# Kernel tuning notes

Hardware: AMD Instinct MI355X
Metric: run time of the kernel (lower is better)

The kernel has to match this reference:

```python
import jax, jax.numpy as jnp
import numpy as np

N, L, H, D = 4, 8192, 8, 64  # batch, seq len, heads, per-head dim
DIM = H * D


def _log_exp_kernel(x):
    # log(1 + exp(x)) positive feature map (softplus)
    return jax.nn.softplus(x)


def setup_inputs() -> dict:
    key = jax.random.key(0)
    k0, k1, k2, k3, k4 = jax.random.split(key, 5)
    s = 1.0 / np.sqrt(DIM).astype(np.float32)
    return {
        "query": jax.random.normal(k0, (N, L, DIM), jnp.float32),
        "key": jax.random.normal(k1, (N, L, DIM), jnp.float32),
        "Wq": jax.random.normal(k2, (DIM, DIM), jnp.float32) * s,
        "Wk": jax.random.normal(k3, (DIM, DIM), jnp.float32) * s,
        "Wv": jax.random.normal(k4, (DIM, DIM), jnp.float32) * s,
    }


def _causal_linear_attention(q, k, v):
    # q, k: (N,H,L,D) kernelized features; v: (N,H,L,D)
    # out[t] = (q_t . S_t) / (q_t . z_t), S_t = sum_{s<=t} k_s v_s^T, z_t = sum_{s<=t} k_s
    qs = jnp.moveaxis(q, 2, 0)  # (L,N,H,D)
    ks = jnp.moveaxis(k, 2, 0)
    vs = jnp.moveaxis(v, 2, 0)
    S0 = jnp.zeros((q.shape[0], q.shape[1], q.shape[3], v.shape[3]), q.dtype)
    z0 = jnp.zeros((q.shape[0], q.shape[1], q.shape[3]), q.dtype)

    def step(carry, xs):
        S, z = carry
        qt, kt, vt = xs  # each (N,H,D)
        S = S + kt[..., :, None] * vt[..., None, :]  # (N,H,D,D)
        z = z + kt
        num = jnp.einsum('nhd,nhde->nhe', qt, S)
        den = jnp.einsum('nhd,nhd->nh', qt, z)
        return (S, z), num / den[..., None]

    _, out = jax.lax.scan(step, (S0, z0), (qs, ks, vs))  # out: (L,N,H,D)
    return jnp.moveaxis(out, 0, 2)  # (N,H,L,D)


def reference(query, key, Wq, Wk, Wv):
    n, Lq, dim = query.shape
    # projections (torch Linear, no bias: x @ W.T), kernel applied in forward...
    q = _log_exp_kernel(query @ Wq.T).reshape(n, Lq, H, D).transpose(0, 2, 1, 3)
    k = _log_exp_kernel(key @ Wk.T).reshape(n, Lq, H, D).transpose(0, 2, 1, 3)
    v = (key @ Wv.T).reshape(n, Lq, H, D).transpose(0, 2, 1, 3)
    # ...and again inside _attention_linear (faithful to the source)
    q = _log_exp_kernel(q)
    k = _log_exp_kernel(k)
    att = _causal_linear_attention(q, k, v)  # (N,H,L,D)
    return att.transpose(0, 2, 1, 3).reshape(n, Lq, H * D)
```

## Files before the change

kernel.cpp:

```cpp
#include <hip/hip_runtime.h>


using bf16x8 = __attribute__((ext_vector_type(8))) short;
using u16x8  = __attribute__((ext_vector_type(8))) unsigned short;
using f32x4  = __attribute__((ext_vector_type(4))) float;

#define L_SEQ   8192
#define NCHUNK  128
#define RECB    8448

__device__ __forceinline__ float bf2f(unsigned short u) {
  union { unsigned int i; float f; } c; c.i = ((unsigned int)u) << 16; return c.f;
}
__device__ __forceinline__ unsigned short f2bf(float f) {
  union { float f; unsigned int i; } c; c.f = f;
  unsigned int r = c.i + 0x7fffu + ((c.i >> 16) & 1u);
  return (unsigned short)(r >> 16);
}
__device__ __forceinline__ float sp_(float x) {
  return (x > 20.0f) ? x : __logf(1.0f + __expf(x));
}
__device__ __forceinline__ void gll16(const void* g, void* l) {
  __builtin_amdgcn_global_load_lds(
      (const __attribute__((address_space(1))) unsigned int*)g,
      (__attribute__((address_space(3))) unsigned int*)l, 16, 0, 0);
}

__global__ void cvt_all(const float* __restrict__ q, const float* __restrict__ k,
                        const float* __restrict__ wq, const float* __restrict__ wk,
                        const float* __restrict__ wv,
                        unsigned short* __restrict__ qo, unsigned short* __restrict__ ko,
                        unsigned short* __restrict__ wqo, unsigned short* __restrict__ wko,
                        unsigned short* __restrict__ wvo) {
  const int stride = gridDim.x * blockDim.x;
  for (int i = blockIdx.x * blockDim.x + threadIdx.x; i < 8585216; i += stride) {
    const float* src; unsigned short* dst; int off;
    if (i < 4194304)      { src = q;  dst = qo;  off = i; }
    else if (i < 8388608) { src = k;  dst = ko;  off = i - 4194304; }
    else if (i < 8454144) { src = wq; dst = wqo; off = i - 8388608; }
    else if (i < 8519680) { src = wk; dst = wko; off = i - 8454144; }
    else                  { src = wv; dst = wvo; off = i - 8519680; }
    float4 v = ((const float4*)src)[off];
    ushort4 o;
    o.x = f2bf(v.x); o.y = f2bf(v.y); o.z = f2bf(v.z); o.w = f2bf(v.w);
    ((ushort4*)dst)[off] = o;
  }
}

__global__ __launch_bounds__(512, 2) void gemm_stream(const unsigned short* __restrict__ qbf,
                                                      const unsigned short* __restrict__ kbf,
                                                      const unsigned short* __restrict__ wqb,
                                                      const unsigned short* __restrict__ wkb,
                                                      const unsigned short* __restrict__ wvb,
                                                      unsigned short* __restrict__ qb,
                                                      unsigned short* __restrict__ kb,
                                                      unsigned short* __restrict__ vt) {
  __shared__ char Ws[131072];
  const int g = blockIdx.x, sub = g >> 8, b = g & 255;
  const int xcd = b & 7, t = b >> 3;
  const int bm = (xcd + (t >> 2) * 8) * 512;
  const int bn = (t & 3) * 128;

  const unsigned short* A; const unsigned short* W; unsigned short* outp; int mode;
  if (sub == 0)      { A = qbf; W = wqb; outp = qb; mode = 0; }
  else if (sub == 1) { A = kbf; W = wkb; outp = kb; mode = 0; }
  else               { A = kbf; W = wvb; outp = vt; mode = 1; }

  const int tid = threadIdx.x, lane = tid & 63, wv = tid >> 6;
  const int l15 = lane & 15, lg = lane >> 4;

  const char* Wb = (const char*)W;
#pragma unroll
  for (int it = 0; it < 16; ++it) {
    const int p = it * 8192 + tid * 16;
    const int col = p >> 10, kb2 = p & 1023;
    gll16(Wb + (size_t)(bn + col) * 1024 + (kb2 ^ ((col & 7) << 4)),
          Ws + it * 8192 + wv * 1024);
  }
  __syncthreads();

  const char* Ab = (const char*)A + (size_t)(bm + wv * 64 + l15) * 1024 + lg * 16;

  f32x4 acc[4][8] = {};
  bf16x8 aC[4], aN[4];
#pragma unroll
  for (int rg = 0; rg < 4; ++rg) aC[rg] = *(const bf16x8*)(Ab + rg * 16384);

#pragma unroll 1
  for (int kk = 0; kk < 16; ++kk) {
    if (kk < 15) {
#pragma unroll
      for (int rg = 0; rg < 4; ++rg)
        aN[rg] = *(const bf16x8*)(Ab + rg * 16384 + (kk + 1) * 64);
    }
    bf16x8 bf[8];
#pragma unroll
    for (int cf = 0; cf < 8; ++cf) {
      const int col = cf * 16 + l15;
      bf[cf] = *(const bf16x8*)(Ws + col * 1024 + ((kk * 64 + lg * 16) ^ ((col & 7) << 4)));
    }
#pragma unroll
    for (int rg = 0; rg < 4; ++rg)
#pragma unroll
      for (int cf = 0; cf < 8; ++cf)
        acc[rg][cf] = __builtin_amdgcn_mfma_f32_16x16x32_bf16(aC[rg], bf[cf], acc[rg][cf], 0, 0, 0);
    if (kk < 15) {
#pragma unroll
      for (int rg = 0; rg < 4; ++rg) aC[rg] = aN[rg];
    }
  }

#pragma unroll
  for (int rg = 0; rg < 4; ++rg)
#pragma unroll
    for (int cf = 0; cf < 8; ++cf)
#pragma unroll
      for (int j = 0; j < 4; ++j) {
        const int m = bm + wv * 64 + rg * 16 + lg * 4 + j;
        const int n = bn + cf * 16 + l15;
        float x = acc[rg][cf][j];
        const int nb = m >> 13;
        const int l  = m & 8191;
        const int h  = n >> 6;
        if (mode == 0) {
          x = sp_(sp_(x));
          const int d = n & 63;
          outp[(((size_t)(nb * 8 + h) * 8192 + l) << 6) + d] = f2bf(x);
        } else {
          const int e = n & 63;
          const int cc = l >> 6, s = l & 63;
          outp[(((size_t)((nb * 8 + h) * 128 + cc) * 64 + e) << 6) + s] = f2bf(x);
        }
      }
}

__global__ __launch_bounds__(256, 4) void chunk_sums(const unsigned short* __restrict__ kb,
                                                     const unsigned short* __restrict__ vt,
                                                     char* __restrict__ S) {
  const int b  = blockIdx.x;
  const int nh = b >> 7, c = b & 127;
  __shared__ char Kt[8192];
  __shared__ char STs[8192];
  const int tid = threadIdx.x, lane = tid & 63, wave = tid >> 6;
  const int l15 = lane & 15, lg = lane >> 4;
  const unsigned short* kch = kb + ((size_t)(nh * L_SEQ + c * 64) << 6);
  const unsigned short* vch = vt + ((size_t)b << 12);

  {
    const int s = tid >> 2, d0 = (tid & 3) << 4;
    u16x8 a = *(const u16x8*)(kch + s * 64 + d0);
    u16x8 bb = *(const u16x8*)(kch + s * 64 + d0 + 8);
#pragma unroll
    for (int i = 0; i < 8; ++i) {
      const int d = d0 + i;
      *(unsigned short*)(Kt + d * 128 + ((2 * s) ^ ((d & 7) << 4))) = a[i];
    }
#pragma unroll
    for (int i = 0; i < 8; ++i) {
      const int d = d0 + 8 + i;
      *(unsigned short*)(Kt + d * 128 + ((2 * s) ^ ((d & 7) << 4))) = bb[i];
    }
  }
  __syncthreads();

  f32x4 acc[4] = {};
#pragma unroll
  for (int kk = 0; kk < 2; ++kk) {
    bf16x8 av = *(const bf16x8*)(vch + (wave * 16 + l15) * 64 + kk * 32 + lg * 8);
#pragma unroll
    for (int ni = 0; ni < 4; ++ni) {
      const int d = ni * 16 + l15;
      bf16x8 bk = *(const bf16x8*)(Kt + d * 128 + ((kk * 64 + lg * 16) ^ ((d & 7) << 4)));
      acc[ni] = __builtin_amdgcn_mfma_f32_16x16x32_bf16(av, bk, acc[ni], 0, 0, 0);
    }
  }

  char* rec = S + (size_t)b * RECB;

  if (tid < 64) {
    float z = 0.f;
#pragma unroll
    for (int kk = 0; kk < 8; ++kk) {
      bf16x8 kv = *(const bf16x8*)(Kt + tid * 128 + ((kk * 16) ^ ((tid & 7) << 4)));
#pragma unroll
      for (int i = 0; i < 8; ++i) z += bf2f(kv[i]);
    }
    *(float*)(rec + 8192 + tid * 4) = z;
  }

#pragma unroll
  for (int ni = 0; ni < 4; ++ni)
#pragma unroll
    for (int j = 0; j < 4; ++j) {
      const int e = wave * 16 + lg * 4 + j, d = ni * 16 + l15;
      *(unsigned short*)(STs + e * 128 + d * 2) = f2bf(acc[ni][j]);
    }
  __syncthreads();
  {
    const int off = tid * 32;
    *(u16x8*)(rec + off)      = *(const u16x8*)(STs + off);
    *(u16x8*)(rec + off + 16) = *(const u16x8*)(STs + off + 16);
  }
}

__global__ void scan_chunks(char* __restrict__ S) {
  const int g = blockIdx.x * 256 + threadIdx.x;
  if (g < 65536) {
    const int nh = g >> 11, pr = g & 2047;
    char* p = S + (size_t)nh * NCHUNK * RECB + pr * 4;
    float a0 = 0.f, a1 = 0.f;
    for (int c = 0; c < NCHUNK; ++c) {
      const unsigned int u = *(unsigned int*)p;
      const float t0 = bf2f((unsigned short)(u & 0xffff));
      const float t1 = bf2f((unsigned short)(u >> 16));
      *(unsigned int*)p = (unsigned int)f2bf(a0) | ((unsigned int)f2bf(a1) << 16);
      a0 += t0; a1 += t1;
      p += RECB;
    }
  } else if (g < 67584) {
    const int idx = g - 65536;
    const int nh = idx >> 6, d = idx & 63;
    char* p = S + (size_t)nh * NCHUNK * RECB + 8192 + d * 4;
    float a = 0.f;
    for (int c = 0; c < NCHUNK; ++c) {
      const float t = *(float*)p; *(float*)p = a; a += t; p += RECB;
    }
  }
}

__global__ __launch_bounds__(256, 2) void attn_out(const unsigned short* __restrict__ qb,
                                                   const unsigned short* __restrict__ kb,
                                                   const unsigned short* __restrict__ vt,
                                                   const char* __restrict__ S,
                                                   float* __restrict__ out) {
  const int b  = blockIdx.x;
  const int nh = b >> 7, c = b & 127;
  const int nb = nh >> 3, h = nh & 7;
  __shared__ char Qs[8192], Ks[8192], Vs[8192], STs[8192], Ps[8192];
  __shared__ float zsh[64], dzh[64];
  const int tid = threadIdx.x, lane = tid & 63, wave = tid >> 6;
  const int l15 = lane & 15, lg = lane >> 4;

  const char* qch = (const char*)(qb + ((size_t)(nh * L_SEQ + c * 64) << 6));
  const char* kch = (const char*)(kb + ((size_t)(nh * L_SEQ + c * 64) << 6));
  const char* vch = (const char*)(vt + ((size_t)b << 12));
  const char* rb  = S + (size_t)b * RECB;

#pragma unroll
  for (int it = 0; it < 2; ++it) {
    const int p  = wave * 2048 + it * 1024 + lane * 16;
    const int r  = p >> 7;
    const int cb = (p & 127) ^ ((r & 7) << 4);
    const int src = r * 128 + cb;
    gll16(qch + src, Qs + wave * 2048 + it * 1024);
    gll16(kch + src, Ks + wave * 2048 + it * 1024);
    gll16(vch + src, Vs + wave * 2048 + it * 1024);
    gll16(rb + src,  STs + wave * 2048 + it * 1024);
  }
  if (tid < 64) zsh[tid] = *(const float*)(rb + 8192 + tid * 4);
  __syncthreads();

  {
    const int t = tid >> 2, p4 = tid & 3;
    float dq = 0.f;
#pragma unroll
    for (int half = 0; half < 2; ++half) {
      const int d0 = p4 * 16 + half * 8;
      const int cb = (d0 * 2) ^ ((t & 7) << 4);
      u16x8 qv = *(const u16x8*)(Qs + t * 128 + cb);
#pragma unroll
      for (int i = 0; i < 8; ++i) dq += bf2f(qv[i]) * zsh[d0 + i];
    }
    dq += __shfl_xor(dq, 1);
    dq += __shfl_xor(dq, 2);
    if (p4 == 0) dzh[t] = dq;
  }
  __syncthreads();

  f32x4 accA[4] = {};
#pragma unroll
  for (int kk = 0; kk < 2; ++kk) {
    const int cb = kk * 64 + lg * 16;
    const int rq = wave * 16 + l15;
    bf16x8 aq = *(const bf16x8*)(Qs + rq * 128 + (cb ^ ((rq & 7) << 4)));
#pragma unroll
    for (int ni = 0; ni < 4; ++ni) {
      const int rk = ni * 16 + l15;
      bf16x8 bk = *(const bf16x8*)(Ks + rk * 128 + (cb ^ ((rk & 7) << 4)));
      accA[ni] = __builtin_amdgcn_mfma_f32_16x16x32_bf16(aq, bk, accA[ni], 0, 0, 0);
    }
  }

  float den4[4];
#pragma unroll
  for (int j = 0; j < 4; ++j) {
    const int t = wave * 16 + lg * 4 + j;
    float rs = 0.f;
#pragma unroll
    for (int ni = 0; ni < 4; ++ni) {
      const int s = ni * 16 + l15;
      const float v = (s <= t) ? accA[ni][j] : 0.f;
      const unsigned short pb = f2bf(v);
      rs += bf2f(pb);
      *(unsigned short*)(Ps + t * 128 + ((s * 2) ^ ((t & 7) << 4))) = pb;
    }
    rs += __shfl_xor(rs, 1);
    rs += __shfl_xor(rs, 2);
    rs += __shfl_xor(rs, 4);
    rs += __shfl_xor(rs, 8);
    den4[j] = rs + dzh[t];
  }
  __syncthreads();

  f32x4 accO[4] = {};
#pragma unroll
  for (int kk = 0; kk < 2; ++kk) {
    const int cb = kk * 64 + lg * 16;
    const int rp = wave * 16 + l15;
    bf16x8 ap = *(const bf16x8*)(Ps + rp * 128 + (cb ^ ((rp & 7) << 4)));
    bf16x8 aq = *(const bf16x8*)(Qs + rp * 128 + (cb ^ ((rp & 7) << 4)));
#pragma unroll
    for (int ni = 0; ni < 4; ++ni) {
      const int rv = ni * 16 + l15;
      bf16x8 bv = *(const bf16x8*)(Vs + rv * 128 + (cb ^ ((rv & 7) << 4)));
      bf16x8 bs = *(const bf16x8*)(STs + rv * 128 + (cb ^ ((rv & 7) << 4)));
      accO[ni] = __builtin_amdgcn_mfma_f32_16x16x32_bf16(ap, bv, accO[ni], 0, 0, 0);
      accO[ni] = __builtin_amdgcn_mfma_f32_16x16x32_bf16(aq, bs, accO[ni], 0, 0, 0);
    }
  }

#pragma unroll
  for (int ni = 0; ni < 4; ++ni) {
    const int e = ni * 16 + l15;
#pragma unroll
    for (int j = 0; j < 4; ++j) {
      const int t = wave * 16 + lg * 4 + j;
      out[((size_t)(nb * L_SEQ + c * 64 + t) << 9) + h * 64 + e] = accO[ni][j] / den4[j];
    }
  }
}

extern "C" void kernel_launch(void* const* d_in, const int* in_sizes, int n_in,
                              void* d_out, int out_size, void* d_ws, size_t ws_size,
                              hipStream_t stream) {
  (void)in_sizes; (void)n_in; (void)out_size; (void)ws_size;
  const float* query = (const float*)d_in[0];
  const float* key   = (const float*)d_in[1];
  const float* Wq    = (const float*)d_in[2];
  const float* Wk    = (const float*)d_in[3];
  const float* Wv    = (const float*)d_in[4];
  float* out = (float*)d_out;
  char* ws = (char*)d_ws;

  unsigned short* qb  = (unsigned short*)(ws);
  unsigned short* kb  = (unsigned short*)(ws + 33554432);
  unsigned short* vt  = (unsigned short*)(ws + 67108864);
  unsigned short* qbf = (unsigned short*)(ws + 100663296);
  unsigned short* kbf = (unsigned short*)(ws + 134217728);
  char*           Ssum = ws + 100663296;
  unsigned short* wqb = (unsigned short*)(ws + 168820736);
  unsigned short* wkb = (unsigned short*)(ws + 169345024);
  unsigned short* wvb = (unsigned short*)(ws + 169869312);

  cvt_all<<<dim3(2048), dim3(256), 0, stream>>>(query, key, Wq, Wk, Wv, qbf, kbf, wqb, wkb, wvb);

  gemm_stream<<<dim3(768), dim3(512), 0, stream>>>(qbf, kbf, wqb, wkb, wvb, qb, kb, vt);

  chunk_sums<<<dim3(4096), dim3(256), 0, stream>>>(kb, vt, Ssum);
  scan_chunks<<<dim3(264), dim3(256), 0, stream>>>(Ssum);
  attn_out<<<dim3(4096), dim3(256), 0, stream>>>(qb, kb, vt, Ssum, out);
}
```

Baseline: 233.8 us.

## Replace projection GEMM with 256x256 tiled, double-buffered LDS pipelined kernel

The old projection GEMM kept a whole 128-column slice of W resident in LDS and streamed A straight from global memory into registers. The new kernel uses 256x256 output tiles and loads both A and W through swizzled LDS buffers with global_load_lds. It double-buffers over the K dimension in eight steps and splits each step into four phases with explicit vmcnt waits, barriers and setprio around the MFMA bursts. It also remaps block IDs across XCDs. Occupancy drops to one 512-thread block per CU, so the kernel relies on the software pipeline rather than on multiple resident blocks to hide latency.

```diff
diff --git a/kernel.cpp b/kernel.cpp
--- a/kernel.cpp
+++ b/kernel.cpp
@@ -47,78 +47,113 @@
   }
 }
 
-__global__ __launch_bounds__(512, 2) void gemm_stream(const unsigned short* __restrict__ qbf,
-                                                      const unsigned short* __restrict__ kbf,
-                                                      const unsigned short* __restrict__ wqb,
-                                                      const unsigned short* __restrict__ wkb,
-                                                      const unsigned short* __restrict__ wvb,
-                                                      unsigned short* __restrict__ qb,
-                                                      unsigned short* __restrict__ kb,
-                                                      unsigned short* __restrict__ vt) {
-  __shared__ char Ws[131072];
-  const int g = blockIdx.x, sub = g >> 8, b = g & 255;
-  const int xcd = b & 7, t = b >> 3;
-  const int bm = (xcd + (t >> 2) * 8) * 512;
-  const int bn = (t & 3) * 128;
+#define SWZR(r) ((((r) & 3) ^ (((r) >> 2) & 3)))
+
+__global__ __launch_bounds__(512, 1) void gemm8p(const unsigned short* __restrict__ qbf,
+                                                 const unsigned short* __restrict__ kbf,
+                                                 const unsigned short* __restrict__ wqb,
+                                                 const unsigned short* __restrict__ wkb,
+                                                 const unsigned short* __restrict__ wvb,
+                                                 unsigned short* __restrict__ qb,
+                                                 unsigned short* __restrict__ kb,
+                                                 unsigned short* __restrict__ vt) {
+  __shared__ char Lds[131072];
+  const int raw = blockIdx.x;
+  const int wg  = (raw & 7) * 96 + (raw >> 3);
+  const int sub = wg >> 8;
+  const int b   = wg & 255;
+  const int bm  = (b >> 1) * 256;
+  const int bn  = (b & 1) * 256;
 
   const unsigned short* A; const unsigned short* W; unsigned short* outp; int mode;
   if (sub == 0)      { A = qbf; W = wqb; outp = qb; mode = 0; }
   else if (sub == 1) { A = kbf; W = wkb; outp = kb; mode = 0; }
   else               { A = kbf; W = wvb; outp = vt; mode = 1; }
-
-  const int tid = threadIdx.x, lane = tid & 63, wv = tid >> 6;
+  const char* Abytes = (const char*)A;
+  const char* Wbytes = (const char*)W;
+
+  const int tid = threadIdx.x, lane = tid & 63, wid = tid >> 6;
   const int l15 = lane & 15, lg = lane >> 4;
-
-  const char* Wb = (const char*)W;
-#pragma unroll
-  for (int it = 0; it < 16; ++it) {
-    const int p = it * 8192 + tid * 16;
-    const int col = p >> 10, kb2 = p & 1023;
-    gll16(Wb + (size_t)(bn + col) * 1024 + (kb2 ^ ((col & 7) << 4)),
-          Ws + it * 8192 + wv * 1024);
-  }
-  __syncthreads();
-
-  const char* Ab = (const char*)A + (size_t)(bm + wv * 64 + l15) * 1024 + lg * 16;
-
-  f32x4 acc[4][8] = {};
-  bf16x8 aC[4], aN[4];
-#pragma unroll
-  for (int rg = 0; rg < 4; ++rg) aC[rg] = *(const bf16x8*)(Ab + rg * 16384);
+  const int wm = wid >> 2, wn = wid & 3;
+
+  f32x4 acc[8][4] = {};
+  bf16x8 bC[4];
+
+#define STG(base, rowbase, tt, h, sl)                                              \
+  { _Pragma("unroll")                                                              \
+    for (int s_ = 0; s_ < 2; ++s_) {                                               \
+      const int r_ = s_ * 128 + (tid >> 2);                                        \
+      const int c_ = ((tid & 3) ^ SWZR(r_)) << 4;                                  \
+      gll16(base + (size_t)(rowbase + r_) * 1024 + (tt) * 128 + (h) * 64 + c_,     \
+            Lds + (sl) * 16384 + s_ * 8192 + wid * 1024);                          \
+    } }
+
+#define LDF(sl, row) \
+  (*(const bf16x8*)(Lds + (sl) * 16384 + (row) * 64 + ((lg ^ SWZR(row)) << 4)))
+
+#define PHASE(bs, ns, t, P, LASTT)                                                    \
+  {                                                                                   \
+    constexpr int mh_ = (P) & 1, kh_ = (P) >> 1;                                      \
+    bf16x8 af[4];                                                                     \
+    _Pragma("unroll")                                                                 \
+    for (int mi = 0; mi < 4; ++mi)                                                    \
+      af[mi] = LDF((bs) + kh_ * 2, wm * 128 + mh_ * 64 + mi * 16 + l15);              \
+    if (mh_ == 0) {                                                                   \
+      _Pragma("unroll")                                                               \
+      for (int ni = 0; ni < 4; ++ni)                                                  \
+        bC[ni] = LDF((bs) + kh_ * 2 + 1, wn * 64 + ni * 16 + l15);                    \
+    }                                                                                 \
+    if (!(LASTT)) {                                                                   \
+      if (mh_) { STG(Wbytes, bn, (t) + 1, kh_, (ns) + kh_ * 2 + 1); }                 \
+      else     { STG(Abytes, bm, (t) + 1, kh_, (ns) + kh_ * 2); }                     \
+    }                                                                                 \
+    if ((LASTT) && (P) == 0) { asm volatile("s_waitcnt vmcnt(0)" ::: "memory"); }     \
+    else                     { asm volatile("s_waitcnt vmcnt(4)" ::: "memory"); }     \
+    __builtin_amdgcn_s_barrier();                                                     \
+    __builtin_amdgcn_s_setprio(1);                                                    \
+    _Pragma("unroll")                                                                 \
+    for (int mi = 0; mi < 4; ++mi)                                                    \
+      _Pragma("unroll")                                                               \
+      for (int ni = 0; ni < 4; ++ni)                                                  \
+        acc[mh_ * 4 + mi][ni] =                                                       \
+            __builtin_amdgcn_mfma_f32_16x16x32_bf16(af[mi], bC[ni],                   \
+                                                    acc[mh_ * 4 + mi][ni], 0, 0, 0);  \
+    __builtin_amdgcn_s_setprio(0);                                                    \
+    __builtin_amdgcn_s_barrier();                                                     \
+  }
+
+  STG(Abytes, bm, 0, 0, 0);
+  STG(Wbytes, bn, 0, 0, 1);
+  STG(Abytes, bm, 0, 1, 2);
+  STG(Wbytes, bn, 0, 1, 3);
+  asm volatile("s_waitcnt vmcnt(4)" ::: "memory");
+  __builtin_amdgcn_s_barrier();
 
 #pragma unroll 1
-  for (int kk = 0; kk < 16; ++kk) {
-    if (kk < 15) {
-#pragma unroll
-      for (int rg = 0; rg < 4; ++rg)
-        aN[rg] = *(const bf16x8*)(Ab + rg * 16384 + (kk + 1) * 64);
-    }
-    bf16x8 bf[8];
-#pragma unroll
-    for (int cf = 0; cf < 8; ++cf) {
-      const int col = cf * 16 + l15;
-      bf[cf] = *(const bf16x8*)(Ws + col * 1024 + ((kk * 64 + lg * 16) ^ ((col & 7) << 4)));
-    }
-#pragma unroll
-    for (int rg = 0; rg < 4; ++rg)
-#pragma unroll
-      for (int cf = 0; cf < 8; ++cf)
-        acc[rg][cf] = __builtin_amdgcn_mfma_f32_16x16x32_bf16(aC[rg], bf[cf], acc[rg][cf], 0, 0, 0);
-    if (kk < 15) {
-#pragma unroll
-      for (int rg = 0; rg < 4; ++rg) aC[rg] = aN[rg];
-    }
-  }
-
-#pragma unroll
-  for (int rg = 0; rg < 4; ++rg)
-#pragma unroll
-    for (int cf = 0; cf < 8; ++cf)
+  for (int t = 0; t < 6; t += 2) {
+    PHASE(0, 4, t, 0, false) PHASE(0, 4, t, 1, false)
+    PHASE(0, 4, t, 2, false) PHASE(0, 4, t, 3, false)
+    PHASE(4, 0, t + 1, 0, false) PHASE(4, 0, t + 1, 1, false)
+    PHASE(4, 0, t + 1, 2, false) PHASE(4, 0, t + 1, 3, false)
+  }
+  PHASE(0, 4, 6, 0, false) PHASE(0, 4, 6, 1, false)
+  PHASE(0, 4, 6, 2, false) PHASE(0, 4, 6, 3, false)
+  PHASE(4, 0, 7, 0, true)  PHASE(4, 0, 7, 1, true)
+  PHASE(4, 0, 7, 2, true)  PHASE(4, 0, 7, 3, true)
+
+#undef PHASE
+#undef LDF
+#undef STG
+
+#pragma unroll
+  for (int am = 0; am < 8; ++am)
+#pragma unroll
+    for (int ni = 0; ni < 4; ++ni)
 #pragma unroll
       for (int j = 0; j < 4; ++j) {
-        const int m = bm + wv * 64 + rg * 16 + lg * 4 + j;
-        const int n = bn + cf * 16 + l15;
-        float x = acc[rg][cf][j];
+        const int m = bm + wm * 128 + am * 16 + lg * 4 + j;
+        const int n = bn + wn * 64 + ni * 16 + l15;
+        float x = acc[am][ni][j];
         const int nb = m >> 13;
         const int l  = m & 8191;
         const int h  = n >> 6;
@@ -364,7 +399,7 @@
 
   cvt_all<<<dim3(2048), dim3(256), 0, stream>>>(query, key, Wq, Wk, Wv, qbf, kbf, wqb, wkb, wvb);
 
-  gemm_stream<<<dim3(768), dim3(512), 0, stream>>>(qbf, kbf, wqb, wkb, wvb, qb, kb, vt);
+  gemm8p<<<dim3(768), dim3(512), 0, stream>>>(qbf, kbf, wqb, wkb, wvb, qb, kb, vt);
 
   chunk_sums<<<dim3(4096), dim3(256), 0, stream>>>(kb, vt, Ssum);
   scan_chunks<<<dim3(264), dim3(256), 0, stream>>>(Ssum);
```

Result: slower. 243.3 us (+4.1%).
